# Kernel optimization log

Measured on AMD Instinct MI355X. Metric: run time of the kernel, lower is better.

## Reference

```python
import jax, jax.numpy as jnp
import numpy as np

S, B, T, A = 512, 64, 768, 512
H1 = (T + T) // 2   # 768
H2 = (T + A) // 2   # 640


def setup_inputs() -> dict:
    key = jax.random.key(0)
    ks = jax.random.split(key, 11)
    sc = 0.02
    return {
        "text": jax.random.normal(ks[0], (B, T), jnp.float32),
        "anp": jax.random.normal(ks[1], (B, A), jnp.float32),
        "text_seq": jax.random.normal(ks[2], (S, B, T), jnp.float32),
        "W11": jax.random.normal(ks[3], (2 * T, H1), jnp.float32) * sc,
        "b11": jax.random.normal(ks[4], (H1,), jnp.float32) * sc,
        "W21": jax.random.normal(ks[5], (H1, 1), jnp.float32) * sc,
        "b21": jax.random.normal(ks[6], (1,), jnp.float32) * sc,
        "W12": jax.random.normal(ks[7], (T + A, H2), jnp.float32) * sc,
        "b12": jax.random.normal(ks[8], (H2,), jnp.float32) * sc,
        "W22": jax.random.normal(ks[9], (H2, 1), jnp.float32) * sc,
        "b22": jax.random.normal(ks[10], (1,), jnp.float32) * sc,
    }


def reference(text, anp, text_seq, W11, b11, W21, b21, W12, b12, W22, b22):
    t = text_seq.shape[-1]
    # cat([text_seq[i], text]) @ W11 == text_seq @ W11[:t] + text @ W11[t:]
    h1 = jnp.tanh(jnp.einsum("sbt,th->sbh", text_seq, W11[:t]) + text @ W11[t:] + b11)
    h2 = jnp.tanh(jnp.einsum("sbt,th->sbh", text_seq, W12[:t]) + anp @ W12[t:] + b12)
    s1 = h1 @ W21 + b21            # (S, B, 1)
    s2 = h2 @ W22 + b22            # (S, B, 1)
    w1 = jax.nn.softmax(s1, axis=0)
    w2 = jax.nn.softmax(s2, axis=0)
    return jnp.mean((w1 + w2) * text_seq * 0.5, axis=0)  # (B, T)
```

## Files before the change

### kernel.cpp

```cpp
#include <hip/hip_runtime.h>
#include <stdint.h>

#define S_DIM 512
#define B_DIM 64
#define T_DIM 768
#define A_DIM 512
#define H1_DIM 768
#define H2_DIM 640
#define N_DIM (H1_DIM + H2_DIM)
#define M_DIM (S_DIM * B_DIM)
#define K_DIM T_DIM
#define NSLOT 22

typedef short s16x8 __attribute__((ext_vector_type(8)));
typedef float f32x4 __attribute__((ext_vector_type(4)));

__device__ __forceinline__ unsigned short f2bf(float f) {
    unsigned u = __float_as_uint(f);
    u += 0x7fffu + ((u >> 16) & 1u);
    return (unsigned short)(u >> 16);
}

#define BIAS_BLKS  (22 * B_DIM)
#define CONVW_BLKS (22 * 12)
#define CONVA_BLKS (M_DIM * K_DIM / 4 / 1024)

__global__ __launch_bounds__(256) void prep_kernel(const float* __restrict__ ts,
                                                   const float* __restrict__ text,
                                                   const float* __restrict__ anp,
                                                   const float* __restrict__ W11,
                                                   const float* __restrict__ b11,
                                                   const float* __restrict__ W12,
                                                   const float* __restrict__ b12,
                                                   unsigned short* __restrict__ Abf,
                                                   unsigned short* __restrict__ Bt,
                                                   float* __restrict__ cbias) {
    const int blk = blockIdx.x;
    __shared__ float lds[64 * 65];
    if (blk < BIAS_BLKS) {
        const int chunk = blk % 22;
        const int b     = blk / 22;
        const int nl    = threadIdx.x & 63;
        const int kg    = threadIdx.x >> 6;
        float a0 = 0.f, a1 = 0.f;
        if (chunk < 12) {
            const int n = chunk * 64 + nl;
            const float* w = W11 + (size_t)T_DIM * H1_DIM + n;
            const float* x = text + b * T_DIM;
            for (int k = kg; k < T_DIM; k += 8) {
                a0 = fmaf(x[k],     w[(size_t)k * H1_DIM],       a0);
                a1 = fmaf(x[k + 4], w[(size_t)(k + 4) * H1_DIM], a1);
            }
        } else {
            const int n2 = (chunk - 12) * 64 + nl;
            const float* w = W12 + (size_t)T_DIM * H2_DIM + n2;
            const float* x = anp + b * A_DIM;
            for (int k = kg; k < A_DIM; k += 8) {
                a0 = fmaf(x[k],     w[(size_t)k * H2_DIM],       a0);
                a1 = fmaf(x[k + 4], w[(size_t)(k + 4) * H2_DIM], a1);
            }
        }
        lds[kg * 64 + nl] = a0 + a1;
        __syncthreads();
        if (kg == 0) {
            const int n = chunk < 12 ? chunk * 64 + nl : H1_DIM + (chunk - 12) * 64 + nl;
            float base = (chunk < 12) ? b11[n] : b12[n - H1_DIM];
            cbias[b * N_DIM + n] =
                base + ((lds[nl] + lds[64 + nl]) + (lds[128 + nl] + lds[192 + nl]));
        }
    } else if (blk < BIAS_BLKS + CONVW_BLKS) {
        const int t  = blk - BIAS_BLKS;
        const int nt = t / 12, kt = t % 12;
        const int n0 = nt * 64, k0 = kt * 64;
        const int lo = threadIdx.x & 63;
        const int hi = threadIdx.x >> 6;
        const float* Wp;  int ld;
        if (nt < 12) { Wp = W11 + n0;            ld = H1_DIM; }
        else         { Wp = W12 + (n0 - H1_DIM); ld = H2_DIM; }
        #pragma unroll
        for (int r = 0; r < 16; ++r) {
            int kl = hi * 16 + r;
            lds[kl * 65 + lo] = Wp[(size_t)(k0 + kl) * ld + lo];
        }
        __syncthreads();
        #pragma unroll
        for (int r = 0; r < 16; ++r) {
            int nl = hi * 16 + r;
            Bt[(size_t)(n0 + nl) * K_DIM + k0 + lo] = f2bf(lds[lo * 65 + nl]);
        }
    } else {
        int i0 = (blk - BIAS_BLKS - CONVW_BLKS) * 1024 + threadIdx.x;
        float4 v0 = ((const float4*)ts)[i0];
        float4 v1 = ((const float4*)ts)[i0 + 256];
        float4 v2 = ((const float4*)ts)[i0 + 512];
        float4 v3 = ((const float4*)ts)[i0 + 768];
        ushort4 o0, o1, o2, o3;
        o0.x = f2bf(v0.x); o0.y = f2bf(v0.y); o0.z = f2bf(v0.z); o0.w = f2bf(v0.w);
        o1.x = f2bf(v1.x); o1.y = f2bf(v1.y); o1.z = f2bf(v1.z); o1.w = f2bf(v1.w);
        o2.x = f2bf(v2.x); o2.y = f2bf(v2.y); o2.z = f2bf(v2.z); o2.w = f2bf(v2.w);
        o3.x = f2bf(v3.x); o3.y = f2bf(v3.y); o3.z = f2bf(v3.z); o3.w = f2bf(v3.w);
        ((ushort4*)Abf)[i0]       = o0;
        ((ushort4*)Abf)[i0 + 256] = o1;
        ((ushort4*)Abf)[i0 + 512] = o2;
        ((ushort4*)Abf)[i0 + 768] = o3;
    }
}

#define BM 128
#define BN 128
#define BK 64

__global__ __launch_bounds__(256, 3) void gemm_score_kernel(
        const unsigned short* __restrict__ A,
        const unsigned short* __restrict__ Bt,
        const float* __restrict__ cbias,
        const float* __restrict__ W21,
        const float* __restrict__ W22,
        float* __restrict__ part) {
    __shared__ __align__(16) unsigned short As[BM * BK];
    __shared__ __align__(16) unsigned short Bs[BN * BK];
    const int tid  = threadIdx.x;
    const int lb   = blockIdx.x;
    const int xcd  = lb & 7;
    const int ib   = lb >> 3;
    const int m0   = ((ib / 11) * 8 + xcd) * BM;
    const int n0   = (ib % 11) * BN;
    const int lane = tid & 63;
    const int wave = tid >> 6;
    const int wm   = wave & 1;
    const int wn   = wave >> 1;
    const int quad = lane >> 4;
    const int col  = lane & 15;
    const int cswz = col & 7;

    f32x4 acc[4][4] = {};

    const int wrow = lane >> 3;
    const int kof  = (((lane & 7) ^ wrow) & 7) * 8;

    for (int k0 = 0; k0 < K_DIM; k0 += BK) {
        #pragma unroll
        for (int p = 0; p < 4; ++p) {
            const int r0 = p * 32 + wave * 8;
            __builtin_amdgcn_global_load_lds(
                (__attribute__((address_space(1))) void*)&A[(size_t)(m0 + r0 + wrow) * K_DIM + k0 + kof],
                (__attribute__((address_space(3))) void*)&As[r0 * BK],
                16, 0, 0);
            __builtin_amdgcn_global_load_lds(
                (__attribute__((address_space(1))) void*)&Bt[(size_t)(n0 + r0 + wrow) * K_DIM + k0 + kof],
                (__attribute__((address_space(3))) void*)&Bs[r0 * BK],
                16, 0, 0);
        }
        __syncthreads();
        #pragma unroll
        for (int kk = 0; kk < BK; kk += 32) {
            s16x8 af[4], bf[4];
            const int ch = ((kk >> 3) + quad) ^ cswz;
            #pragma unroll
            for (int i = 0; i < 4; ++i)
                af[i] = *(const s16x8*)&As[(wm * 64 + i * 16 + col) * BK + ch * 8];
            #pragma unroll
            for (int j = 0; j < 4; ++j)
                bf[j] = *(const s16x8*)&Bs[(wn * 64 + j * 16 + col) * BK + ch * 8];
            #pragma unroll
            for (int i = 0; i < 4; ++i)
                #pragma unroll
                for (int j = 0; j < 4; ++j)
                    acc[i][j] = __builtin_amdgcn_mfma_f32_16x16x32_bf16(af[i], bf[j], acc[i][j], 0, 0, 0);
        }
        __syncthreads();
    }

    const int half = (n0 >= H1_DIM) ? 1 : 0;
    const int jb   = n0 >> 7;
    const float* w2p = half ? (W22 - H1_DIM) : W21;
    int   ncol[4];
    float w2v[4];
    #pragma unroll
    for (int j = 0; j < 4; ++j) {
        ncol[j] = n0 + wn * 64 + j * 16 + col;
        w2v[j]  = w2p[ncol[j]];
    }
    float* pc = part + (jb * 2 + wn) * M_DIM;
    #pragma unroll
    for (int i = 0; i < 4; ++i) {
        #pragma unroll
        for (int r = 0; r < 4; ++r) {
            int row_local = wm * 64 + i * 16 + quad * 4 + r;
            int b = row_local & (B_DIM - 1);
            int s = (m0 + row_local) >> 6;
            float v = 0.f;
            #pragma unroll
            for (int j = 0; j < 4; ++j) {
                float pre = acc[i][j][r] + cbias[b * N_DIM + ncol[j]];
                float ex  = __expf(2.f * pre);
                float th  = 1.f - 2.f * __builtin_amdgcn_rcpf(ex + 1.f);
                v = fmaf(th, w2v[j], v);
            }
            v += __shfl_xor(v, 1);
            v += __shfl_xor(v, 2);
            v += __shfl_xor(v, 4);
            v += __shfl_xor(v, 8);
            if (col == 0) pc[b * S_DIM + s] = v;
        }
    }
}

__global__ __launch_bounds__(512) void softmax_kernel(const float* __restrict__ part,
                                                      float* __restrict__ wsum) {
    const int b = blockIdx.x, s = threadIdx.x;
    __shared__ float redm[16], reds[16];
    float v0 = 0.f, v1 = 0.f;
    #pragma unroll
    for (int sl = 0; sl < 12; ++sl)       v0 += part[sl * M_DIM + b * S_DIM + s];
    #pragma unroll
    for (int sl = 12; sl < NSLOT; ++sl)   v1 += part[sl * M_DIM + b * S_DIM + s];
    float m0 = v0, m1 = v1;
    #pragma unroll
    for (int off = 32; off > 0; off >>= 1) {
        m0 = fmaxf(m0, __shfl_xor(m0, off));
        m1 = fmaxf(m1, __shfl_xor(m1, off));
    }
    const int w = s >> 6;
    if ((s & 63) == 0) { redm[w] = m0; redm[8 + w] = m1; }
    __syncthreads();
    m0 = redm[0]; m1 = redm[8];
    #pragma unroll
    for (int i = 1; i < 8; ++i) { m0 = fmaxf(m0, redm[i]); m1 = fmaxf(m1, redm[8 + i]); }
    float e0 = expf(v0 - m0), e1 = expf(v1 - m1);
    float s0 = e0, s1 = e1;
    #pragma unroll
    for (int off = 32; off > 0; off >>= 1) {
        s0 += __shfl_xor(s0, off);
        s1 += __shfl_xor(s1, off);
    }
    if ((s & 63) == 0) { reds[w] = s0; reds[8 + w] = s1; }
    __syncthreads();
    s0 = reds[0]; s1 = reds[8];
    #pragma unroll
    for (int i = 1; i < 8; ++i) { s0 += reds[i]; s1 += reds[8 + i]; }
    wsum[b * S_DIM + s] = e0 / s0 + e1 / s1;
}

__global__ __launch_bounds__(128) void wmean_kernel(const unsigned short* __restrict__ Abf,
                                                    const float* __restrict__ wsum,
                                                    float* __restrict__ out) {
    const int b  = blockIdx.x;
    const int tp = blockIdx.y * 128 + threadIdx.x;
    const int s0 = blockIdx.z * 128;
    const unsigned short* base = Abf + (size_t)b * T_DIM + tp * 2;
    const float* wp = wsum + b * S_DIM;
    float a0 = 0.f, a1 = 0.f, c0 = 0.f, c1 = 0.f;
    #pragma unroll 4
    for (int s = s0; s < s0 + 128; s += 2) {
        float w0 = wp[s], w1 = wp[s + 1];
        unsigned u0 = *(const unsigned*)(base + (size_t)s * (B_DIM * T_DIM));
        unsigned u1 = *(const unsigned*)(base + (size_t)(s + 1) * (B_DIM * T_DIM));
        a0 = fmaf(w0, __uint_as_float(u0 << 16),          a0);
        a1 = fmaf(w0, __uint_as_float(u0 & 0xffff0000u),  a1);
        c0 = fmaf(w1, __uint_as_float(u1 << 16),          c0);
        c1 = fmaf(w1, __uint_as_float(u1 & 0xffff0000u),  c1);
    }
    atomicAdd(&out[b * T_DIM + tp * 2],     (a0 + c0) * (0.5f / (float)S_DIM));
    atomicAdd(&out[b * T_DIM + tp * 2 + 1], (a1 + c1) * (0.5f / (float)S_DIM));
}

extern "C" void kernel_launch(void* const* d_in, const int* in_sizes, int n_in,
                              void* d_out, int out_size, void* d_ws, size_t ws_size,
                              hipStream_t stream) {
    const float* text = (const float*)d_in[0];
    const float* anp  = (const float*)d_in[1];
    const float* ts   = (const float*)d_in[2];
    const float* W11  = (const float*)d_in[3];
    const float* b11  = (const float*)d_in[4];
    const float* W21  = (const float*)d_in[5];
    const float* W12  = (const float*)d_in[7];
    const float* b12  = (const float*)d_in[8];
    const float* W22  = (const float*)d_in[9];
    float* out = (float*)d_out;

    char* ws = (char*)d_ws;
    unsigned short* Abf = (unsigned short*)ws;
    unsigned short* Bt  = (unsigned short*)(ws + 50331648);
    float* cbias = (float*)(ws + 50331648 + 2162688);
    float* part  = (float*)(ws + 50331648 + 2162688 + 360448);
    float* wsum  = (float*)(ws + 50331648 + 2162688 + 360448 + 2883584);

    hipMemsetAsync(out, 0, B_DIM * T_DIM * sizeof(float), stream);
    prep_kernel<<<BIAS_BLKS + CONVW_BLKS + CONVA_BLKS, 256, 0, stream>>>(
        ts, text, anp, W11, b11, W12, b12, Abf, Bt, cbias);
    gemm_score_kernel<<<(M_DIM / BM) * (N_DIM / BN), 256, 0, stream>>>(
        Abf, Bt, cbias, W21, W22, part);
    softmax_kernel<<<B_DIM, 512, 0, stream>>>(part, wsum);
    wmean_kernel<<<dim3(B_DIM, 3, 4), 128, 0, stream>>>(Abf, wsum, out);
}
```

Before: 297.1 us.

## Enlarge GEMM tiles to 256x256 with multi-buffered LDS pipeline and padded N

Rewrites the fused GEMM+score kernel to use 256x256 tiles with 512 threads, triple-buffered A and double-buffered B in dynamic LDS, and explicit vmcnt waits so global loads overlap MFMA work. It also raises wave priority around MFMA bursts. N is padded from 1408 to 1536 with zeroed weights and bias so it divides evenly into 256-wide tiles, and the partial-score layout changes to row-major by m. The padding adds wasted MFMA work, and the large LDS footprint limits occupancy.

```diff
diff --git a/kernel.cpp b/kernel.cpp
--- a/kernel.cpp
+++ b/kernel.cpp
@@ -7,10 +7,11 @@
 #define A_DIM 512
 #define H1_DIM 768
 #define H2_DIM 640
-#define N_DIM (H1_DIM + H2_DIM)
-#define M_DIM (S_DIM * B_DIM)
-#define K_DIM T_DIM
-#define NSLOT 22
+#define N_REAL 1408
+#define NPAD   1536
+#define M_DIM  (S_DIM * B_DIM)
+#define K_DIM  T_DIM
+#define NSLOT  24
 
 typedef short s16x8 __attribute__((ext_vector_type(8)));
 typedef float f32x4 __attribute__((ext_vector_type(4)));
@@ -21,8 +22,8 @@
     return (unsigned short)(u >> 16);
 }
 
-#define BIAS_BLKS  (22 * B_DIM)
-#define CONVW_BLKS (22 * 12)
+#define BIAS_BLKS  (24 * B_DIM)
+#define CONVW_BLKS (24 * 12)
 #define CONVA_BLKS (M_DIM * K_DIM / 4 / 1024)
 
 __global__ __launch_bounds__(256) void prep_kernel(const float* __restrict__ ts,
@@ -38,8 +39,13 @@
     const int blk = blockIdx.x;
     __shared__ float lds[64 * 65];
     if (blk < BIAS_BLKS) {
-        const int chunk = blk % 22;
-        const int b     = blk / 22;
+        const int chunk = blk % 24;
+        const int b     = blk / 24;
+        if (chunk >= 22) {
+            if (threadIdx.x < 64)
+                cbias[b * NPAD + N_REAL + (chunk - 22) * 64 + threadIdx.x] = 0.f;
+            return;
+        }
         const int nl    = threadIdx.x & 63;
         const int kg    = threadIdx.x >> 6;
         float a0 = 0.f, a1 = 0.f;
@@ -65,7 +71,7 @@
         if (kg == 0) {
             const int n = chunk < 12 ? chunk * 64 + nl : H1_DIM + (chunk - 12) * 64 + nl;
             float base = (chunk < 12) ? b11[n] : b12[n - H1_DIM];
-            cbias[b * N_DIM + n] =
+            cbias[b * NPAD + n] =
                 base + ((lds[nl] + lds[64 + nl]) + (lds[128 + nl] + lds[192 + nl]));
         }
     } else if (blk < BIAS_BLKS + CONVW_BLKS) {
@@ -74,6 +80,12 @@
         const int n0 = nt * 64, k0 = kt * 64;
         const int lo = threadIdx.x & 63;
         const int hi = threadIdx.x >> 6;
+        if (nt >= 22) {
+            #pragma unroll
+            for (int r = 0; r < 16; ++r)
+                Bt[(size_t)(n0 + hi * 16 + r) * K_DIM + k0 + lo] = 0;
+            return;
+        }
         const float* Wp;  int ld;
         if (nt < 12) { Wp = W11 + n0;            ld = H1_DIM; }
         else         { Wp = W12 + (n0 - H1_DIM); ld = H2_DIM; }
@@ -106,93 +118,167 @@
     }
 }
 
-#define BM 128
-#define BN 128
+#define BM 256
+#define BN 256
 #define BK 64
-
-__global__ __launch_bounds__(256, 3) void gemm_score_kernel(
+#define GEMM_LDS 163840
+
+#define BARX()  __builtin_amdgcn_s_barrier()
+#define VMC4()  asm volatile("s_waitcnt vmcnt(4)" ::: "memory")
+#define VMC0()  asm volatile("s_waitcnt vmcnt(0)" ::: "memory")
+
+__global__ __launch_bounds__(512, 2) void gemm_score_kernel(
         const unsigned short* __restrict__ A,
         const unsigned short* __restrict__ Bt,
         const float* __restrict__ cbias,
         const float* __restrict__ W21,
         const float* __restrict__ W22,
         float* __restrict__ part) {
-    __shared__ __align__(16) unsigned short As[BM * BK];
-    __shared__ __align__(16) unsigned short Bs[BN * BK];
+    extern __shared__ __align__(16) char smem[];
+    unsigned short* lds16 = (unsigned short*)smem;
+
     const int tid  = threadIdx.x;
     const int lb   = blockIdx.x;
-    const int xcd  = lb & 7;
-    const int ib   = lb >> 3;
-    const int m0   = ((ib / 11) * 8 + xcd) * BM;
-    const int n0   = (ib % 11) * BN;
+    const int gid  = (lb & 7) * 96 + (lb >> 3);
+    const int mt   = gid / 6;
+    const int nt   = gid % 6;
+    const int m0   = mt * BM;
+    const int n0   = nt * BN;
     const int lane = tid & 63;
     const int wave = tid >> 6;
     const int wm   = wave & 1;
     const int wn   = wave >> 1;
     const int quad = lane >> 4;
     const int col  = lane & 15;
-    const int cswz = col & 7;
-
-    f32x4 acc[4][4] = {};
-
-    const int wrow = lane >> 3;
-    const int kof  = (((lane & 7) ^ wrow) & 7) * 8;
-
-    for (int k0 = 0; k0 < K_DIM; k0 += BK) {
-        #pragma unroll
-        for (int p = 0; p < 4; ++p) {
-            const int r0 = p * 32 + wave * 8;
-            __builtin_amdgcn_global_load_lds(
-                (__attribute__((address_space(1))) void*)&A[(size_t)(m0 + r0 + wrow) * K_DIM + k0 + kof],
-                (__attribute__((address_space(3))) void*)&As[r0 * BK],
-                16, 0, 0);
-            __builtin_amdgcn_global_load_lds(
-                (__attribute__((address_space(1))) void*)&Bt[(size_t)(n0 + r0 + wrow) * K_DIM + k0 + kof],
-                (__attribute__((address_space(3))) void*)&Bs[r0 * BK],
-                16, 0, 0);
-        }
-        __syncthreads();
-        #pragma unroll
-        for (int kk = 0; kk < BK; kk += 32) {
-            s16x8 af[4], bf[4];
-            const int ch = ((kk >> 3) + quad) ^ cswz;
-            #pragma unroll
-            for (int i = 0; i < 4; ++i)
-                af[i] = *(const s16x8*)&As[(wm * 64 + i * 16 + col) * BK + ch * 8];
+
+    const int srow = tid >> 3;
+    const int sko  = ((tid & 7) ^ (srow & 7)) * 8;
+    const unsigned short* gA = A  + (size_t)(m0 + srow) * K_DIM + sko;
+    const unsigned short* gB = Bt + (size_t)(n0 + srow) * K_DIM + sko;
+    const int ldsw = wave * 1024;
+
+    int arow[4], brow[4];
+    #pragma unroll
+    for (int ii = 0; ii < 4; ++ii) arow[ii] = (ii * 32 + wm * 16 + col) * BK;
+    #pragma unroll
+    for (int j = 0; j < 4; ++j)  brow[j] = (wn * 64 + j * 16 + col) * BK;
+    const int c0 = (quad ^ (col & 7)) * 8;
+    const int c1 = ((4 + quad) ^ (col & 7)) * 8;
+
+    f32x4 acc[8][4] = {};
+
+    auto stageA = [&](int buf, int kt) {
+        #pragma unroll
+        for (int h = 0; h < 2; ++h)
+            #pragma unroll
+            for (int i = 0; i < 2; ++i)
+                __builtin_amdgcn_global_load_lds(
+                    (__attribute__((address_space(1))) void*)(gA + (size_t)(h * 128 + i * 64) * K_DIM + kt * BK),
+                    (__attribute__((address_space(3))) void*)(smem + buf * 32768 + h * 16384 + i * 8192 + ldsw),
+                    16, 0, 0);
+    };
+    auto stageB = [&](int buf, int kt) {
+        #pragma unroll
+        for (int h = 0; h < 2; ++h)
+            #pragma unroll
+            for (int i = 0; i < 2; ++i)
+                __builtin_amdgcn_global_load_lds(
+                    (__attribute__((address_space(1))) void*)(gB + (size_t)(h * 128 + i * 64) * K_DIM + kt * BK),
+                    (__attribute__((address_space(3))) void*)(smem + 98304 + buf * 32768 + h * 16384 + i * 8192 + ldsw),
+                    16, 0, 0);
+    };
+
+    stageA(0, 0);
+    stageB(0, 0);
+    stageA(1, 1);
+    VMC4();
+    BARX();
+
+    int ab = 0, bb = 0;
+    #pragma unroll 1
+    for (int t = 0; t < 12; ++t) {
+        const unsigned short* Ab = lds16 + ab * 16384;
+        const unsigned short* Bb = lds16 + 49152 + bb * 16384;
+        s16x8 af[4], ag[4], bf[4];
+
+        #pragma unroll
+        for (int ii = 0; ii < 4; ++ii) af[ii] = *(const s16x8*)&Ab[arow[ii] + c0];
+        #pragma unroll
+        for (int j = 0; j < 4; ++j)  bf[j] = *(const s16x8*)&Bb[brow[j] + c0];
+        if (t < 11) stageB(bb ^ 1, t + 1);
+        BARX();
+        __builtin_amdgcn_s_setprio(1);
+        #pragma unroll
+        for (int ii = 0; ii < 4; ++ii)
             #pragma unroll
             for (int j = 0; j < 4; ++j)
-                bf[j] = *(const s16x8*)&Bs[(wn * 64 + j * 16 + col) * BK + ch * 8];
-            #pragma unroll
-            for (int i = 0; i < 4; ++i)
-                #pragma unroll
-                for (int j = 0; j < 4; ++j)
-                    acc[i][j] = __builtin_amdgcn_mfma_f32_16x16x32_bf16(af[i], bf[j], acc[i][j], 0, 0, 0);
-        }
-        __syncthreads();
-    }
-
-    const int half = (n0 >= H1_DIM) ? 1 : 0;
-    const int jb   = n0 >> 7;
-    const float* w2p = half ? (W22 - H1_DIM) : W21;
-    int   ncol[4];
-    float w2v[4];
+                acc[ii][j] = __builtin_amdgcn_mfma_f32_16x16x32_bf16(af[ii], bf[j], acc[ii][j], 0, 0, 0);
+        __builtin_amdgcn_s_setprio(0);
+        BARX();
+
+        #pragma unroll
+        for (int ii = 0; ii < 4; ++ii) ag[ii] = *(const s16x8*)&Ab[8192 + arow[ii] + c0];
+        if (t < 10) { int a2 = ab ? ab - 1 : 2; stageA(a2, t + 2); }
+        BARX();
+        __builtin_amdgcn_s_setprio(1);
+        #pragma unroll
+        for (int ii = 0; ii < 4; ++ii)
+            #pragma unroll
+            for (int j = 0; j < 4; ++j)
+                acc[4 + ii][j] = __builtin_amdgcn_mfma_f32_16x16x32_bf16(ag[ii], bf[j], acc[4 + ii][j], 0, 0, 0);
+        __builtin_amdgcn_s_setprio(0);
+        BARX();
+
+        #pragma unroll
+        for (int ii = 0; ii < 4; ++ii) af[ii] = *(const s16x8*)&Ab[arow[ii] + c1];
+        #pragma unroll
+        for (int j = 0; j < 4; ++j)  bf[j] = *(const s16x8*)&Bb[brow[j] + c1];
+        BARX();
+        __builtin_amdgcn_s_setprio(1);
+        #pragma unroll
+        for (int ii = 0; ii < 4; ++ii)
+            #pragma unroll
+            for (int j = 0; j < 4; ++j)
+                acc[ii][j] = __builtin_amdgcn_mfma_f32_16x16x32_bf16(af[ii], bf[j], acc[ii][j], 0, 0, 0);
+        __builtin_amdgcn_s_setprio(0);
+        BARX();
+
+        #pragma unroll
+        for (int ii = 0; ii < 4; ++ii) ag[ii] = *(const s16x8*)&Ab[8192 + arow[ii] + c1];
+        if (t < 10) { VMC4(); } else { VMC0(); }
+        BARX();
+        __builtin_amdgcn_s_setprio(1);
+        #pragma unroll
+        for (int ii = 0; ii < 4; ++ii)
+            #pragma unroll
+            for (int j = 0; j < 4; ++j)
+                acc[4 + ii][j] = __builtin_amdgcn_mfma_f32_16x16x32_bf16(ag[ii], bf[j], acc[4 + ii][j], 0, 0, 0);
+        __builtin_amdgcn_s_setprio(0);
+        BARX();
+
+        ab = (ab == 2) ? 0 : ab + 1;
+        bb ^= 1;
+    }
+
+    const int slot = nt * 4 + wn;
+    float w2v[4]; int ncj[4];
     #pragma unroll
     for (int j = 0; j < 4; ++j) {
-        ncol[j] = n0 + wn * 64 + j * 16 + col;
-        w2v[j]  = w2p[ncol[j]];
-    }
-    float* pc = part + (jb * 2 + wn) * M_DIM;
-    #pragma unroll
-    for (int i = 0; i < 4; ++i) {
+        int nc = n0 + wn * 64 + j * 16 + col;
+        ncj[j] = nc;
+        w2v[j] = (nc < H1_DIM) ? W21[nc] : (nc < N_REAL ? W22[nc - H1_DIM] : 0.f);
+    }
+    float* pc = part + (size_t)slot * M_DIM + m0;
+    #pragma unroll
+    for (int i = 0; i < 8; ++i) {
         #pragma unroll
         for (int r = 0; r < 4; ++r) {
-            int row_local = wm * 64 + i * 16 + quad * 4 + r;
-            int b = row_local & (B_DIM - 1);
-            int s = (m0 + row_local) >> 6;
+            const int row_local = (i >> 2) * 128 + (i & 3) * 32 + wm * 16 + quad * 4 + r;
+            const int b = row_local & (B_DIM - 1);
             float v = 0.f;
             #pragma unroll
             for (int j = 0; j < 4; ++j) {
-                float pre = acc[i][j][r] + cbias[b * N_DIM + ncol[j]];
+                float pre = acc[i][j][r] + cbias[b * NPAD + ncj[j]];
                 float ex  = __expf(2.f * pre);
                 float th  = 1.f - 2.f * __builtin_amdgcn_rcpf(ex + 1.f);
                 v = fmaf(th, w2v[j], v);
@@ -201,7 +287,7 @@
             v += __shfl_xor(v, 2);
             v += __shfl_xor(v, 4);
             v += __shfl_xor(v, 8);
-            if (col == 0) pc[b * S_DIM + s] = v;
+            if (col == 0) pc[row_local] = v;
         }
     }
 }
@@ -210,16 +296,17 @@
                                                       float* __restrict__ wsum) {
     const int b = blockIdx.x, s = threadIdx.x;
     __shared__ float redm[16], reds[16];
+    const size_t off = (size_t)s * 64 + b;
     float v0 = 0.f, v1 = 0.f;
     #pragma unroll
-    for (int sl = 0; sl < 12; ++sl)       v0 += part[sl * M_DIM + b * S_DIM + s];
-    #pragma unroll
-    for (int sl = 12; sl < NSLOT; ++sl)   v1 += part[sl * M_DIM + b * S_DIM + s];
+    for (int sl = 0; sl < 12; ++sl)       v0 += part[(size_t)sl * M_DIM + off];
+    #pragma unroll
+    for (int sl = 12; sl < NSLOT; ++sl)   v1 += part[(size_t)sl * M_DIM + off];
     float m0 = v0, m1 = v1;
     #pragma unroll
-    for (int off = 32; off > 0; off >>= 1) {
-        m0 = fmaxf(m0, __shfl_xor(m0, off));
-        m1 = fmaxf(m1, __shfl_xor(m1, off));
+    for (int offx = 32; offx > 0; offx >>= 1) {
+        m0 = fmaxf(m0, __shfl_xor(m0, offx));
+        m1 = fmaxf(m1, __shfl_xor(m1, offx));
     }
     const int w = s >> 6;
     if ((s & 63) == 0) { redm[w] = m0; redm[8 + w] = m1; }
@@ -230,9 +317,9 @@
     float e0 = expf(v0 - m0), e1 = expf(v1 - m1);
     float s0 = e0, s1 = e1;
     #pragma unroll
-    for (int off = 32; off > 0; off >>= 1) {
-        s0 += __shfl_xor(s0, off);
-        s1 += __shfl_xor(s1, off);
+    for (int offx = 32; offx > 0; offx >>= 1) {
+        s0 += __shfl_xor(s0, offx);
+        s1 += __shfl_xor(s1, offx);
     }
     if ((s & 63) == 0) { reds[w] = s0; reds[8 + w] = s1; }
     __syncthreads();
@@ -282,14 +369,21 @@
     char* ws = (char*)d_ws;
     unsigned short* Abf = (unsigned short*)ws;
     unsigned short* Bt  = (unsigned short*)(ws + 50331648);
-    float* cbias = (float*)(ws + 50331648 + 2162688);
-    float* part  = (float*)(ws + 50331648 + 2162688 + 360448);
-    float* wsum  = (float*)(ws + 50331648 + 2162688 + 360448 + 2883584);
+    float* cbias = (float*)(ws + 52690944);
+    float* part  = (float*)(ws + 53084160);
+    float* wsum  = (float*)(ws + 56229888);
+
+    static int lds_attr_set = 0;
+    if (!lds_attr_set) {
+        hipFuncSetAttribute((const void*)gemm_score_kernel,
+                            hipFuncAttributeMaxDynamicSharedMemorySize, GEMM_LDS);
+        lds_attr_set = 1;
+    }
 
     hipMemsetAsync(out, 0, B_DIM * T_DIM * sizeof(float), stream);
     prep_kernel<<<BIAS_BLKS + CONVW_BLKS + CONVA_BLKS, 256, 0, stream>>>(
         ts, text, anp, W11, b11, W12, b12, Abf, Bt, cbias);
-    gemm_score_kernel<<<(M_DIM / BM) * (N_DIM / BN), 256, 0, stream>>>(
+    gemm_score_kernel<<<(M_DIM / BM) * (NPAD / BN), 512, GEMM_LDS, stream>>>(
         Abf, Bt, cbias, W21, W22, part);
     softmax_kernel<<<B_DIM, 512, 0, stream>>>(part, wsum);
     wmean_kernel<<<dim3(B_DIM, 3, 4), 128, 0, stream>>>(Abf, wsum, out);
```

New measurement: 330.1 us. +11.1%, slower.
